# Kernel optimization log

Hardware: AMD Instinct MI355X
Metric: run time of the kernel (lower is better)

Reference implementation:

```python
import jax, jax.numpy as jnp
import numpy as np

TOP_K = 5
THRESHOLD = 0.0
EPS = 1e-12

def l2_normalize(x, axis):
    sq = jnp.sum(x * x, axis=axis, keepdims=True)
    return x * jax.lax.rsqrt(jnp.maximum(sq, EPS))

def setup_inputs() -> dict:
    key = jax.random.key(0)
    k1, k2, k3, k4 = jax.random.split(key, 4)
    B, S, D = 256, 197, 768
    P, L, T = 20, 5, 10
    x_embed = jax.random.normal(k1, (B, S, D), dtype=jnp.float32)
    prompt = jax.random.uniform(k2, (P, L, D), dtype=jnp.float32, minval=-1.0, maxval=1.0)
    prompt_key = jax.random.uniform(k3, (P, D), dtype=jnp.float32, minval=-1.0, maxval=1.0)
    assist_prompt = jax.random.uniform(k4, (T, L, D), dtype=jnp.float32, minval=-1.0, maxval=1.0)
    return {"x_embed": x_embed, "prompt": prompt, "prompt_key": prompt_key,
            "assist_prompt": assist_prompt, "test": 0}

def reference(x_embed, prompt, prompt_key, assist_prompt, test):
    B = x_embed.shape[0]
    D = x_embed.shape[-1]
    # embedding key: mean over tokens
    x_mean = jnp.mean(x_embed, axis=1)                 # [B, D]
    x_norm = l2_normalize(x_mean, axis=1)              # [B, D]  (test >= 0 branch)
    p_norm = l2_normalize(prompt_key, axis=1)          # [P, D]
    similarity = x_norm @ p_norm.T                     # [B, P]
    vals, idx = jax.lax.top_k(similarity, TOP_K)       # sorted descending -> pruning mask is a prefix
    keep = vals > THRESHOLD                            # [B, K]
    idx_pruned = jnp.where(keep, idx, -1)              # [B, K], -1 = dummy prompt
    idx_safe = jnp.maximum(idx_pruned, 0)
    # gather selected prompts, zero-out pruned slots (dummy prompts)
    sel = jnp.where(keep[:, :, None, None], prompt[idx_safe], 0.0)     # [B, K, L, D]
    assist_b = jnp.broadcast_to(assist_prompt, (B,) + assist_prompt.shape)  # [B, T, L, D]
    selected = jnp.concatenate([assist_b, sel], axis=1)                # [B, T+K, L, D]
    tokens = selected.reshape(B, -1, D)                                # [B, (T+K)*L, D]
    # reduce_sim: sum over all valid (b,k) keys of key . x_b', summed over b', / B
    gathered_keys = jnp.where(keep[:, :, None], p_norm[idx_safe], 0.0) # [B, K, D]
    key_total = jnp.sum(gathered_keys, axis=(0, 1))                    # [D]
    reduce_sim = jnp.dot(jnp.sum(x_norm, axis=0), key_total) / B
    prompted_embedding = jnp.concatenate([tokens, x_embed], axis=1)    # [B, (T+K)*L + S, D]
    return prompted_embedding, reduce_sim, tokens, idx_pruned, x_norm
```

## Files before the change

kernel.cpp:

```cpp
#include <hip/hip_runtime.h>

#define B 256
#define S 197
#define D 768
#define P 20
#define L 5
#define T 10
#define K 5

#define ROWS_PE 272
#define SZ_PE   (B * ROWS_PE * D)
#define OFF_RS  ((long)SZ_PE)
#define OFF_TOK (OFF_RS + 1)
#define SZ_TOK  (B * (T + K) * L * D)
#define OFF_IDX (OFF_TOK + SZ_TOK)
#define OFF_XN  (OFF_IDX + B * K)

__global__ void k_mean_copy(const float* __restrict__ x, float* __restrict__ pe,
                            float* __restrict__ partial) {
    const int tile = blockIdx.x;
    const int b = blockIdx.y;
    const int t = threadIdx.x;
    const int s0 = tile * 50;
    const int s1 = (s0 + 50 < S) ? s0 + 50 : S;
    const float4* x4 = (const float4*)x;
    float4* o4 = (float4*)pe;
    const int xbase = (b * S) * (D / 4) + t;
    const int obase = (b * ROWS_PE + (T + K) * L) * (D / 4) + t;
    float4 acc = make_float4(0.f, 0.f, 0.f, 0.f);
    for (int s = s0; s < s1; ++s) {
        float4 v = x4[xbase + s * (D / 4)];
        acc.x += v.x; acc.y += v.y; acc.z += v.z; acc.w += v.w;
        o4[obase + s * (D / 4)] = v;
    }
    ((float4*)partial)[(b * 4 + tile) * (D / 4) + t] = acc;
}

__global__ void k_simtopk(const float* __restrict__ partial, const float* __restrict__ pkey,
                          float* __restrict__ xnorm_out, float* __restrict__ xsum,
                          float* __restrict__ idxp_f, int* __restrict__ idx_ws,
                          int* __restrict__ keycnt) {
    const int b = blockIdx.x;
    const int t = threadIdx.x;
    const int lane = t & 63, wid = t >> 6;
    __shared__ float xs[D];
    __shared__ float sim[P];
    __shared__ float red[4];

    float v0 = 0.f, v1 = 0.f, v2 = 0.f;
    for (int tile = 0; tile < 4; ++tile) {
        const float* p = partial + (b * 4 + tile) * D;
        v0 += p[t]; v1 += p[t + 256]; v2 += p[t + 512];
    }
    const float invS = 1.0f / (float)S;
    v0 *= invS; v1 *= invS; v2 *= invS;
    float ss = v0 * v0 + v1 * v1 + v2 * v2;
    for (int o = 32; o > 0; o >>= 1) ss += __shfl_down(ss, o);
    if (lane == 0) red[wid] = ss;
    __syncthreads();
    if (t == 0) red[0] = rsqrtf(fmaxf(red[0] + red[1] + red[2] + red[3], 1e-12f));
    __syncthreads();
    const float r = red[0];
    v0 *= r; v1 *= r; v2 *= r;
    xs[t] = v0; xs[t + 256] = v1; xs[t + 512] = v2;
    xnorm_out[b * D + t] = v0;
    xnorm_out[b * D + t + 256] = v1;
    xnorm_out[b * D + t + 512] = v2;
    atomicAdd(&xsum[t], v0);
    atomicAdd(&xsum[t + 256], v1);
    atomicAdd(&xsum[t + 512], v2);
    __syncthreads();

    for (int p = wid; p < P; p += 4) {
        const float* pr = pkey + p * D;
        float axk = 0.f, akk = 0.f;
        for (int d = lane; d < D; d += 64) {
            const float kv = pr[d];
            axk += xs[d] * kv;
            akk += kv * kv;
        }
        for (int o = 32; o > 0; o >>= 1) {
            axk += __shfl_down(axk, o);
            akk += __shfl_down(akk, o);
        }
        if (lane == 0) sim[p] = axk * rsqrtf(fmaxf(akk, 1e-12f));
    }
    __syncthreads();
    if (t == 0) {
        bool used[P];
        for (int p = 0; p < P; ++p) used[p] = false;
        for (int k = 0; k < K; ++k) {
            float best = -INFINITY; int bi = 0;
            for (int p = 0; p < P; ++p)
                if (!used[p] && sim[p] > best) { best = sim[p]; bi = p; }
            used[bi] = true;
            const int oi = (best > 0.0f) ? bi : -1;
            idxp_f[b * K + k] = (float)oi;
            idx_ws[b * K + k] = oi;
            if (oi >= 0) atomicAdd(&keycnt[bi], 1);
        }
    }
}

__global__ void k_tokens(const float* __restrict__ prompt, const float* __restrict__ assist,
                         const int* __restrict__ idx_ws, float* __restrict__ pe,
                         float* __restrict__ tok) {
    const int j = blockIdx.x;
    const int b = blockIdx.y;
    const int t = threadIdx.x;
    float4 v;
    if (j < T * L) {
        v = ((const float4*)(assist + j * D))[t];
    } else {
        const int k = (j - T * L) / L, l = (j - T * L) % L;
        const int idx = idx_ws[b * K + k];
        if (idx < 0) v = make_float4(0.f, 0.f, 0.f, 0.f);
        else         v = ((const float4*)(prompt + (idx * L + l) * D))[t];
    }
    ((float4*)(pe + (long)(b * ROWS_PE + j) * D))[t] = v;
    float* d2 = tok + (long)(b * (T + K) * L + j) * D + 4 * t;
    d2[0] = v.x; d2[1] = v.y; d2[2] = v.z; d2[3] = v.w;
}

__global__ void k_reduce(const float* __restrict__ xsum, const float* __restrict__ pkey,
                         const int* __restrict__ keycnt, float* __restrict__ rs) {
    const int t = threadIdx.x;
    const int lane = t & 63, wid = t >> 6;
    __shared__ float coef[P];
    __shared__ float red[4];
    for (int p = wid; p < P; p += 4) {
        const float* pr = pkey + p * D;
        float akk = 0.f;
        for (int d = lane; d < D; d += 64) { const float kv = pr[d]; akk += kv * kv; }
        for (int o = 32; o > 0; o >>= 1) akk += __shfl_down(akk, o);
        if (lane == 0) coef[p] = (float)keycnt[p] * rsqrtf(fmaxf(akk, 1e-12f));
    }
    __syncthreads();
    float acc = 0.f;
    for (int c = 0; c < 3; ++c) {
        const int d = t + c * 256;
        float kt = 0.f;
        for (int p = 0; p < P; ++p) kt += coef[p] * pkey[p * D + d];
        acc += xsum[d] * kt;
    }
    for (int o = 32; o > 0; o >>= 1) acc += __shfl_down(acc, o);
    if (lane == 0) red[wid] = acc;
    __syncthreads();
    if (t == 0) rs[0] = (red[0] + red[1] + red[2] + red[3]) * (1.0f / (float)B);
}

extern "C" void kernel_launch(void* const* d_in, const int* in_sizes, int n_in,
                              void* d_out, int out_size, void* d_ws, size_t ws_size,
                              hipStream_t stream) {
    const float* x      = (const float*)d_in[0];
    const float* prompt = (const float*)d_in[1];
    const float* pkey   = (const float*)d_in[2];
    const float* assist = (const float*)d_in[3];
    float* out = (float*)d_out;
    float* ws = (float*)d_ws;

    float* partial = ws;
    int*   keycnt  = (int*)(partial + B * 4 * D);
    float* xsum    = (float*)(keycnt + P);
    int*   idx_ws  = (int*)(xsum + D);

    hipMemsetAsync(keycnt, 0, (P + D) * sizeof(float), stream);

    k_mean_copy<<<dim3(4, B), 192, 0, stream>>>(x, out, partial);
    k_simtopk<<<B, 256, 0, stream>>>(partial, pkey, out + OFF_XN, xsum,
                                     out + OFF_IDX, idx_ws, keycnt);
    k_tokens<<<dim3((T + K) * L, B), 192, 0, stream>>>(prompt, assist, idx_ws, out, out + OFF_TOK);
    k_reduce<<<1, 256, 0, stream>>>(xsum, pkey, keycnt, out + OFF_RS);
}
```

Baseline: 463.4 us.

## Fuse similarity, token gather and reduce into one kernel with last-block reduction

Merges the top-k, token gather and reduce_sim kernels into a single launch. Extra blocks write the assist tokens, and each batch block writes its own selected prompts. The final reduce runs in whichever block finishes last, detected through an atomic counter. Copies use nontemporal loads and stores, and the mean-copy grid is flattened to 1D. This removes two launches and the round trip through a workspace index buffer, at the cost of relying on correct atomic and fence ordering for the last-block pattern.

```diff
diff --git a/kernel.cpp b/kernel.cpp
--- a/kernel.cpp
+++ b/kernel.cpp
@@ -16,41 +16,67 @@
 #define OFF_IDX (OFF_TOK + SZ_TOK)
 #define OFF_XN  (OFF_IDX + B * K)
 
-__global__ void k_mean_copy(const float* __restrict__ x, float* __restrict__ pe,
-                            float* __restrict__ partial) {
-    const int tile = blockIdx.x;
-    const int b = blockIdx.y;
+typedef float f4 __attribute__((ext_vector_type(4)));
+
+__global__ void __launch_bounds__(192)
+k_mean_copy(const float* __restrict__ x, float* __restrict__ pe,
+            float* __restrict__ partial) {
+    const int tile = blockIdx.x & 3;
+    const int b = blockIdx.x >> 2;
     const int t = threadIdx.x;
     const int s0 = tile * 50;
     const int s1 = (s0 + 50 < S) ? s0 + 50 : S;
-    const float4* x4 = (const float4*)x;
-    float4* o4 = (float4*)pe;
-    const int xbase = (b * S) * (D / 4) + t;
+    const f4* x4 = (const f4*)x;
+    f4* o4 = (f4*)pe;
+    const int xbase = b * S * (D / 4) + t;
     const int obase = (b * ROWS_PE + (T + K) * L) * (D / 4) + t;
-    float4 acc = make_float4(0.f, 0.f, 0.f, 0.f);
+    f4 acc = {0.f, 0.f, 0.f, 0.f};
     for (int s = s0; s < s1; ++s) {
-        float4 v = x4[xbase + s * (D / 4)];
-        acc.x += v.x; acc.y += v.y; acc.z += v.z; acc.w += v.w;
-        o4[obase + s * (D / 4)] = v;
-    }
-    ((float4*)partial)[(b * 4 + tile) * (D / 4) + t] = acc;
+        f4 v = __builtin_nontemporal_load(x4 + xbase + s * (D / 4));
+        acc += v;
+        __builtin_nontemporal_store(v, o4 + obase + s * (D / 4));
+    }
+    ((f4*)partial)[blockIdx.x * (D / 4) + t] = acc;
 }
 
-__global__ void k_simtopk(const float* __restrict__ partial, const float* __restrict__ pkey,
-                          float* __restrict__ xnorm_out, float* __restrict__ xsum,
-                          float* __restrict__ idxp_f, int* __restrict__ idx_ws,
-                          int* __restrict__ keycnt) {
+__global__ void __launch_bounds__(256)
+k_fuse(const float* __restrict__ partial, const float* __restrict__ pkey,
+       const float* __restrict__ prompt, const float* __restrict__ assist,
+       float* __restrict__ pe, float* __restrict__ tok,
+       float* __restrict__ xnorm_out, float* __restrict__ idxp_f,
+       float* __restrict__ xsum, int* __restrict__ keycnt,
+       unsigned int* __restrict__ done, float* __restrict__ rs) {
+    const int t = threadIdx.x;
+
+    if (blockIdx.x >= B) {
+        const int item = (blockIdx.x - B) * 256 + t;
+        const int b = item / 9600;
+        const int r = item - b * 9600;
+        const int j = r / 192;
+        const int c = r - j * 192;
+        const f4 v = ((const f4*)assist)[j * 192 + c];
+        __builtin_nontemporal_store(v, (f4*)pe + ((long)b * ROWS_PE + j) * 192 + c);
+        float* d2 = tok + ((long)b * 75 + j) * 768 + 4 * c;
+        __builtin_nontemporal_store(v[0], d2 + 0);
+        __builtin_nontemporal_store(v[1], d2 + 1);
+        __builtin_nontemporal_store(v[2], d2 + 2);
+        __builtin_nontemporal_store(v[3], d2 + 3);
+        return;
+    }
+
     const int b = blockIdx.x;
-    const int t = threadIdx.x;
     const int lane = t & 63, wid = t >> 6;
     __shared__ float xs[D];
     __shared__ float sim[P];
     __shared__ float red[4];
+    __shared__ float coef[P];
+    __shared__ int sidx[K];
+    __shared__ int amLast;
 
     float v0 = 0.f, v1 = 0.f, v2 = 0.f;
     for (int tile = 0; tile < 4; ++tile) {
-        const float* p = partial + (b * 4 + tile) * D;
-        v0 += p[t]; v1 += p[t + 256]; v2 += p[t + 512];
+        const float* pp = partial + (b * 4 + tile) * D;
+        v0 += pp[t]; v1 += pp[t + 256]; v2 += pp[t + 512];
     }
     const float invS = 1.0f / (float)S;
     v0 *= invS; v1 *= invS; v2 *= invS;
@@ -60,8 +86,8 @@
     __syncthreads();
     if (t == 0) red[0] = rsqrtf(fmaxf(red[0] + red[1] + red[2] + red[3], 1e-12f));
     __syncthreads();
-    const float r = red[0];
-    v0 *= r; v1 *= r; v2 *= r;
+    const float rn = red[0];
+    v0 *= rn; v1 *= rn; v2 *= rn;
     xs[t] = v0; xs[t + 256] = v1; xs[t + 512] = v2;
     xnorm_out[b * D + t] = v0;
     xnorm_out[b * D + t + 256] = v1;
@@ -86,67 +112,72 @@
         if (lane == 0) sim[p] = axk * rsqrtf(fmaxf(akk, 1e-12f));
     }
     __syncthreads();
+
     if (t == 0) {
-        bool used[P];
-        for (int p = 0; p < P; ++p) used[p] = false;
+        unsigned usedMask = 0u;
         for (int k = 0; k < K; ++k) {
             float best = -INFINITY; int bi = 0;
             for (int p = 0; p < P; ++p)
-                if (!used[p] && sim[p] > best) { best = sim[p]; bi = p; }
-            used[bi] = true;
+                if (!((usedMask >> p) & 1u) && sim[p] > best) { best = sim[p]; bi = p; }
+            usedMask |= 1u << bi;
             const int oi = (best > 0.0f) ? bi : -1;
+            sidx[k] = oi;
             idxp_f[b * K + k] = (float)oi;
-            idx_ws[b * K + k] = oi;
             if (oi >= 0) atomicAdd(&keycnt[bi], 1);
         }
     }
-}
-
-__global__ void k_tokens(const float* __restrict__ prompt, const float* __restrict__ assist,
-                         const int* __restrict__ idx_ws, float* __restrict__ pe,
-                         float* __restrict__ tok) {
-    const int j = blockIdx.x;
-    const int b = blockIdx.y;
-    const int t = threadIdx.x;
-    float4 v;
-    if (j < T * L) {
-        v = ((const float4*)(assist + j * D))[t];
-    } else {
-        const int k = (j - T * L) / L, l = (j - T * L) % L;
-        const int idx = idx_ws[b * K + k];
-        if (idx < 0) v = make_float4(0.f, 0.f, 0.f, 0.f);
-        else         v = ((const float4*)(prompt + (idx * L + l) * D))[t];
-    }
-    ((float4*)(pe + (long)(b * ROWS_PE + j) * D))[t] = v;
-    float* d2 = tok + (long)(b * (T + K) * L + j) * D + 4 * t;
-    d2[0] = v.x; d2[1] = v.y; d2[2] = v.z; d2[3] = v.w;
-}
-
-__global__ void k_reduce(const float* __restrict__ xsum, const float* __restrict__ pkey,
-                         const int* __restrict__ keycnt, float* __restrict__ rs) {
-    const int t = threadIdx.x;
-    const int lane = t & 63, wid = t >> 6;
-    __shared__ float coef[P];
-    __shared__ float red[4];
-    for (int p = wid; p < P; p += 4) {
-        const float* pr = pkey + p * D;
-        float akk = 0.f;
-        for (int d = lane; d < D; d += 64) { const float kv = pr[d]; akk += kv * kv; }
-        for (int o = 32; o > 0; o >>= 1) akk += __shfl_down(akk, o);
-        if (lane == 0) coef[p] = (float)keycnt[p] * rsqrtf(fmaxf(akk, 1e-12f));
-    }
-    __syncthreads();
-    float acc = 0.f;
-    for (int c = 0; c < 3; ++c) {
-        const int d = t + c * 256;
-        float kt = 0.f;
-        for (int p = 0; p < P; ++p) kt += coef[p] * pkey[p * D + d];
-        acc += xsum[d] * kt;
-    }
-    for (int o = 32; o > 0; o >>= 1) acc += __shfl_down(acc, o);
-    if (lane == 0) red[wid] = acc;
-    __syncthreads();
-    if (t == 0) rs[0] = (red[0] + red[1] + red[2] + red[3]) * (1.0f / (float)B);
+    __syncthreads();
+
+    for (int it = t; it < K * L * 192; it += 256) {
+        const int j = it / 192;
+        const int c = it - j * 192;
+        const int k = j / L;
+        const int l = j - k * L;
+        const int idx = sidx[k];
+        f4 v = {0.f, 0.f, 0.f, 0.f};
+        if (idx >= 0) v = ((const f4*)prompt)[(idx * L + l) * 192 + c];
+        __builtin_nontemporal_store(v, (f4*)pe + ((long)b * ROWS_PE + T * L + j) * 192 + c);
+        float* d2 = tok + ((long)b * 75 + T * L + j) * 768 + 4 * c;
+        __builtin_nontemporal_store(v[0], d2 + 0);
+        __builtin_nontemporal_store(v[1], d2 + 1);
+        __builtin_nontemporal_store(v[2], d2 + 2);
+        __builtin_nontemporal_store(v[3], d2 + 3);
+    }
+
+    if (t == 0) {
+        __threadfence();
+        const unsigned prev =
+            __hip_atomic_fetch_add(done, 1u, __ATOMIC_ACQ_REL, __HIP_MEMORY_SCOPE_AGENT);
+        amLast = (prev == (unsigned)(B - 1)) ? 1 : 0;
+    }
+    __syncthreads();
+    if (amLast) {
+        for (int p = wid; p < P; p += 4) {
+            const float* pr = pkey + p * D;
+            float akk = 0.f;
+            for (int d = lane; d < D; d += 64) { const float kv = pr[d]; akk += kv * kv; }
+            for (int o = 32; o > 0; o >>= 1) akk += __shfl_down(akk, o);
+            if (lane == 0) {
+                const int cnt =
+                    __hip_atomic_load(&keycnt[p], __ATOMIC_RELAXED, __HIP_MEMORY_SCOPE_AGENT);
+                coef[p] = (float)cnt * rsqrtf(fmaxf(akk, 1e-12f));
+            }
+        }
+        __syncthreads();
+        float acc = 0.f;
+        for (int cc = 0; cc < 3; ++cc) {
+            const int d = t + cc * 256;
+            float kt = 0.f;
+            for (int p = 0; p < P; ++p) kt += coef[p] * pkey[p * D + d];
+            const float xv =
+                __hip_atomic_load(&xsum[d], __ATOMIC_RELAXED, __HIP_MEMORY_SCOPE_AGENT);
+            acc += xv * kt;
+        }
+        for (int o = 32; o > 0; o >>= 1) acc += __shfl_down(acc, o);
+        if (lane == 0) red[wid] = acc;
+        __syncthreads();
+        if (t == 0) rs[0] = (red[0] + red[1] + red[2] + red[3]) * (1.0f / (float)B);
+    }
 }
 
 extern "C" void kernel_launch(void* const* d_in, const int* in_sizes, int n_in,
@@ -157,18 +188,18 @@
     const float* pkey   = (const float*)d_in[2];
     const float* assist = (const float*)d_in[3];
     float* out = (float*)d_out;
-    float* ws = (float*)d_ws;
-
-    float* partial = ws;
-    int*   keycnt  = (int*)(partial + B * 4 * D);
-    float* xsum    = (float*)(keycnt + P);
-    int*   idx_ws  = (int*)(xsum + D);
-
-    hipMemsetAsync(keycnt, 0, (P + D) * sizeof(float), stream);
-
-    k_mean_copy<<<dim3(4, B), 192, 0, stream>>>(x, out, partial);
-    k_simtopk<<<B, 256, 0, stream>>>(partial, pkey, out + OFF_XN, xsum,
-                                     out + OFF_IDX, idx_ws, keycnt);
-    k_tokens<<<dim3((T + K) * L, B), 192, 0, stream>>>(prompt, assist, idx_ws, out, out + OFF_TOK);
-    k_reduce<<<1, 256, 0, stream>>>(xsum, pkey, keycnt, out + OFF_RS);
+    float* ws  = (float*)d_ws;
+
+    float* partial   = ws;
+    int*   keycnt    = (int*)(partial + B * 4 * D);
+    float* xsum      = (float*)(keycnt + P);
+    unsigned* done   = (unsigned*)(xsum + D);
+
+    hipMemsetAsync(keycnt, 0, (P + D + 1) * sizeof(float), stream);
+
+    k_mean_copy<<<dim3(4 * B), 192, 0, stream>>>(x, out, partial);
+    k_fuse<<<dim3(B + 9600), 256, 0, stream>>>(partial, pkey, prompt, assist,
+                                               out, out + OFF_TOK,
+                                               out + OFF_XN, out + OFF_IDX,
+                                               xsum, keycnt, done, out + OFF_RS);
 }
```

Result: faster. 449.8 us (-2.9%).
